# Performance work log

Hardware: AMD Instinct MI355X
Metric: run time of the kernel (lower is better)

Reference implementation:

```python
import jax, jax.numpy as jnp
import numpy as np

N = 20000
E = 640000
R = 8          # num_rels == num_bases (basis regularizer with num_bases=-1)
B = 8
IN_SIZE = 128
HID = 256      # 4 * fea_dimen
FEA = 64
TIME = 2880
POI = 12


def setup_inputs() -> dict:
    key = jax.random.key(0)
    ks = jax.random.split(key, 20)
    s = 0.02
    inp = {
        'src': jax.random.randint(ks[0], (E,), 0, N),
        'dst': jax.random.randint(ks[1], (E,), 0, N),
        'etype': jax.random.randint(ks[2], (E,), 0, R),
        'poi_distribution': jax.random.normal(ks[3], (N, POI), jnp.float32),
        'time_distribution': jax.random.normal(ks[4], (N, TIME), jnp.float32),
        'road_feature': jax.random.normal(ks[5], (N, IN_SIZE), jnp.float32),
        # input projections
        'poi_w': jax.random.normal(ks[6], (POI, FEA), jnp.float32) * s,
        'poi_b': jnp.zeros((FEA,), jnp.float32),
        'time_w': jax.random.normal(ks[7], (TIME, 2 * FEA), jnp.float32) * s,
        'time_b': jnp.zeros((2 * FEA,), jnp.float32),
        'road_w': jax.random.normal(ks[8], (IN_SIZE, FEA), jnp.float32) * s,
        'road_b': jnp.zeros((FEA,), jnp.float32),
        # RelGraphConv layer 1 (basis decomposition)
        'basis1': jax.random.normal(ks[9], (B, HID, HID), jnp.float32) * s,
        'coef1': jax.random.normal(ks[10], (R, B), jnp.float32) * s,
        'loop_w1': jax.random.normal(ks[11], (HID, HID), jnp.float32) * s,
        'bias1': jnp.zeros((HID,), jnp.float32),
        # RelGraphConv layer 2
        'basis2': jax.random.normal(ks[12], (B, HID, HID), jnp.float32) * s,
        'coef2': jax.random.normal(ks[13], (R, B), jnp.float32) * s,
        'loop_w2': jax.random.normal(ks[14], (HID, HID), jnp.float32) * s,
        'bias2': jnp.zeros((HID,), jnp.float32),
    }
    return inp


def _rel_graph_conv(h, src, dst, etype, basis, coef, loop_w, bias):
    # W_r = sum_b coef[r,b] * basis[b]  -> (R, HID, HID), small
    W = jnp.einsum('rb,bio->rio', coef, basis)
    # transform every node by every relation weight, then gather per edge
    y = jnp.einsum('ni,rio->nro', h, W)          # (N, R, HID)
    msgs = y[src, etype]                          # (E, HID) gather
    agg = jax.ops.segment_sum(msgs, dst, num_segments=h.shape[0])  # scatter-sum
    return agg + h @ loop_w + bias


def reference(src, dst, etype, poi_distribution, time_distribution, road_feature,
              poi_w, poi_b, time_w, time_b, road_w, road_b,
              basis1, coef1, loop_w1, bias1, basis2, coef2, loop_w2, bias2):
    poi_feat = poi_distribution @ poi_w + poi_b       # (N, 64)
    time_feat = time_distribution @ time_w + time_b   # (N, 128)
    road_feat = road_feature @ road_w + road_b        # (N, 64)
    feat = jnp.concatenate([poi_feat, time_feat, road_feat], axis=1)  # (N, 256)
    h = _rel_graph_conv(feat, src, dst, etype, basis1, coef1, loop_w1, bias1)
    h = jax.nn.relu(h)  # dropout=0.0 -> identity
    h = _rel_graph_conv(h, src, dst, etype, basis2, coef2, loop_w2, bias2)
    return h
```

## Files before the change

### kernel.cpp

```cpp
#include <hip/hip_runtime.h>

#define NN 20000
#define NE 640000
#define NR 8
#define NB 8
#define HID 256
#define KPOI 12
#define KTIME 2880
#define KROAD 128
#define NK (NN * NR)
#define NS 9
#define KCAT (NS * HID)

typedef __attribute__((ext_vector_type(8))) short bf8_t;
typedef __attribute__((ext_vector_type(4))) float f4_t;

__device__ inline unsigned short f2bf(float f) {
  unsigned int u = __float_as_uint(f);
  u += 0x7FFF + ((u >> 16) & 1);
  return (unsigned short)(u >> 16);
}
__device__ inline float bf2f(unsigned short h) {
  return __uint_as_float((unsigned int)h << 16);
}

__device__ inline void gl_lds16(const void* g, void* l) {
  __builtin_amdgcn_global_load_lds(
      (const __attribute__((address_space(1))) void*)g,
      (__attribute__((address_space(3))) void*)l, 16, 0, 0);
}

#define BK 16
__device__ inline void sgemm_body(
    int M, int Nn, int K,
    const float* __restrict__ A, int lda,
    const float* __restrict__ B, int ldb,
    const float* __restrict__ bias,
    unsigned short* __restrict__ C, int ldc, int brow, char* lds)
{
  constexpr int BM = 64, BN = 64, TM = 4, TN = 4;
  constexpr int SA = BM + 4;
  constexpr int SB = BN + 4;
  float* As = (float*)lds;
  float* Bs = (float*)(lds + 4352);
  const int tid = threadIdx.x;
  constexpr int TCOLS = BN / TN;
  const int row0 = (tid / TCOLS) * TM;
  const int col0 = (tid % TCOLS) * TN;

  float acc[TM][TN] = {};

  for (int kb = 0; kb < K; kb += BK) {
    {
      int i = tid;
      int r = i >> 2, q = (i & 3) * 4;
      int grow = brow + r, gk = kb + q;
      if (grow < M && gk + 3 < K) {
        float4 v = *(const float4*)(A + (size_t)grow * lda + gk);
        As[(q + 0) * SA + r] = v.x;
        As[(q + 1) * SA + r] = v.y;
        As[(q + 2) * SA + r] = v.z;
        As[(q + 3) * SA + r] = v.w;
      } else {
#pragma unroll
        for (int j = 0; j < 4; ++j)
          As[(q + j) * SA + r] =
              (grow < M && gk + j < K) ? A[(size_t)grow * lda + gk + j] : 0.f;
      }
    }
    {
      int i = tid;
      int k = i / (BN / 4), cq = (i % (BN / 4)) * 4;
      int gk = kb + k;
      float4 v = {0.f, 0.f, 0.f, 0.f};
      if (gk < K) {
        if (cq + 3 < Nn) {
          v = *(const float4*)(B + (size_t)gk * ldb + cq);
        } else {
#pragma unroll
          for (int j = 0; j < 4; ++j)
            if (cq + j < Nn) (&v.x)[j] = B[(size_t)gk * ldb + cq + j];
        }
      }
      *(float4*)(&Bs[k * SB + cq]) = v;
    }
    __syncthreads();
#pragma unroll
    for (int kk = 0; kk < BK; ++kk) {
      float a[TM], bb[TN];
      *(float4*)(&a[0]) = *(const float4*)(&As[kk * SA + row0]);
      *(float4*)(&bb[0]) = *(const float4*)(&Bs[kk * SB + col0]);
#pragma unroll
      for (int i = 0; i < TM; ++i)
#pragma unroll
        for (int j = 0; j < TN; ++j)
          acc[i][j] += a[i] * bb[j];
    }
    __syncthreads();
  }

  float bcache[TN];
#pragma unroll
  for (int j = 0; j < TN; ++j) bcache[j] = bias[col0 + j];
#pragma unroll
  for (int i = 0; i < TM; ++i) {
    int row = brow + row0 + i;
    if (row >= M) continue;
#pragma unroll
    for (int j = 0; j < TN; ++j)
      C[(size_t)row * ldc + col0 + j] = f2bf(acc[i][j] + bcache[j]);
  }
}

__global__ __launch_bounds__(256) void hist_prep_k(
    const int* __restrict__ dstp, const int* __restrict__ etp,
    int* __restrict__ counts,
    const float* __restrict__ loop_w1, const float* __restrict__ loop_w2,
    const float* __restrict__ time_w,
    const float* __restrict__ coef1, const float* __restrict__ basis1,
    const float* __restrict__ coef2, const float* __restrict__ basis2,
    const float* __restrict__ poi_dist, const float* __restrict__ poi_w,
    const float* __restrict__ poi_b,
    const float* __restrict__ road_feat, const float* __restrict__ road_w,
    const float* __restrict__ road_b,
    unsigned short* __restrict__ Wc1, unsigned short* __restrict__ Wc2,
    unsigned short* __restrict__ TWT, unsigned short* __restrict__ hbuf)
{
  __shared__ __align__(16) char lds[8704];
  int b = blockIdx.x;
  if (b < 2500) {
    int e = b * 256 + threadIdx.x;
    atomicAdd(&counts[dstp[e] * NR + etp[e]], 1);
    return;
  }
  b -= 2500;
  const int to = threadIdx.x & 63;
  const int tq = threadIdx.x >> 6;

  if (b < 378) {
    unsigned short (*T)[66] = (unsigned short (*)[66])lds;
    if (b < 256) {
      const int lr = b >> 4;
      const int tile = b & 15;
      const int i0 = ((tile >> 2) & 3) * 64, o0 = (tile & 3) * 64;
      const float* coef  = (lr < NR) ? coef1 : coef2;
      const float* basis = (lr < NR) ? basis1 : basis2;
      unsigned short* Wc = (lr < NR) ? Wc1 : Wc2;
      const int r = lr & 7;
      float cf[NB];
#pragma unroll
      for (int q = 0; q < NB; ++q) cf[q] = coef[r * NB + q];
#pragma unroll
      for (int k = 0; k < 16; ++k) {
        int i_loc = tq * 16 + k;
        int i = i0 + i_loc;
        float acc = 0.f;
#pragma unroll
        for (int q = 0; q < NB; ++q)
          acc += cf[q] * basis[((size_t)(q * HID + i)) * HID + o0 + to];
        T[i_loc][to] = f2bf(acc);
      }
      __syncthreads();
#pragma unroll
      for (int k = 0; k < 16; ++k) {
        int o_loc = tq * 16 + k;
        Wc[(size_t)(o0 + o_loc) * KCAT + r * HID + i0 + to] = T[to][o_loc];
      }
    } else if (b < 288) {
      const int j = b - 256;
      const int layer = j >> 4;
      const int tile = j & 15;
      const int i0 = ((tile >> 2) & 3) * 64, o0 = (tile & 3) * 64;
      const float* lw = layer ? loop_w2 : loop_w1;
      unsigned short* Wc = layer ? Wc2 : Wc1;
#pragma unroll
      for (int k = 0; k < 16; ++k) {
        int i_loc = tq * 16 + k;
        T[i_loc][to] = f2bf(lw[(size_t)(i0 + i_loc) * HID + o0 + to]);
      }
      __syncthreads();
#pragma unroll
      for (int k = 0; k < 16; ++k) {
        int o_loc = tq * 16 + k;
        Wc[(size_t)(o0 + o_loc) * KCAT + NR * HID + i0 + to] = T[to][o_loc];
      }
    } else {
      const int j = b - 288;
      const int r0 = (j >> 1) * 64, c0 = (j & 1) * 64;
#pragma unroll
      for (int k = 0; k < 16; ++k) {
        int r_loc = tq * 16 + k;
        T[r_loc][to] = f2bf(time_w[(size_t)(r0 + r_loc) * 128 + c0 + to]);
      }
      __syncthreads();
#pragma unroll
      for (int k = 0; k < 16; ++k) {
        int c_loc = tq * 16 + k;
        TWT[(size_t)(c0 + c_loc) * KTIME + r0 + to] = T[to][c_loc];
      }
    }
  } else if (b < 691) {
    sgemm_body(NN, 64, KPOI, poi_dist, KPOI, poi_w, 64, poi_b,
               hbuf + 0, HID, (b - 378) * 64, lds);
  } else {
    sgemm_body(NN, 64, KROAD, road_feat, KROAD, road_w, 64, road_b,
               hbuf + 192, HID, (b - 691) * 64, lds);
  }
}

__global__ __launch_bounds__(256) void scan_all(
    const int* __restrict__ counts, int* __restrict__ offs,
    int* __restrict__ cursor, int* __restrict__ bsums,
    int* __restrict__ counter) {
  __shared__ int sh[256];
  const int bid = blockIdx.x;
  const int t = threadIdx.x;
  const int nblk = gridDim.x;
  const int gbase = bid * 1024;
  int v[4], run[4];
  int s = 0;
#pragma unroll
  for (int j = 0; j < 4; ++j) {
    int idx = gbase + t * 4 + j;
    v[j] = (idx < NK) ? counts[idx] : 0;
    s += v[j];
  }
  sh[t] = s;
  __syncthreads();
  for (int off = 1; off < 256; off <<= 1) {
    int x = (t >= off) ? sh[t - off] : 0;
    __syncthreads();
    sh[t] += x;
    __syncthreads();
  }
  {
    int r = sh[t] - s;
#pragma unroll
    for (int j = 0; j < 4; ++j) { run[j] = r; r += v[j]; }
  }
  if (t == 255) {
    bsums[bid] = sh[255];
    __threadfence();
    atomicAdd(counter, 1);
  }
  if (t == 0) {
    while (atomicAdd(counter, 0) < nblk) {}
    __threadfence();
  }
  __syncthreads();
  int bs = (t < nblk) ? atomicAdd(&bsums[t], 0) : 0;
  __syncthreads();
  sh[t] = bs;
  __syncthreads();
  for (int off = 1; off < 256; off <<= 1) {
    int x = (t >= off) ? sh[t - off] : 0;
    __syncthreads();
    sh[t] += x;
    __syncthreads();
  }
  const int base = (bid > 0) ? sh[bid - 1] : 0;
#pragma unroll
  for (int j = 0; j < 4; ++j) {
    int idx = gbase + t * 4 + j;
    if (idx < NK) {
      int val = run[j] + base;
      offs[idx] = val;
      cursor[idx] = val;
    }
  }
  if (bid == 0 && t == 0) offs[NK] = NE;
}

__global__ __launch_bounds__(512) void fill_time_k(
    const int* __restrict__ srcp, const int* __restrict__ dstp,
    const int* __restrict__ etp, int* __restrict__ cursor,
    unsigned short* __restrict__ ssrc,
    const float* __restrict__ A,
    const unsigned short* __restrict__ BT,
    const float* __restrict__ bias,
    unsigned short* __restrict__ featb)
{
  __shared__ __align__(16) char lds[40960];
  int b = blockIdx.x;
  if (b < 1250) {
    int e = b * 512 + threadIdx.x;
    int key = dstp[e] * NR + etp[e];
    int p = atomicAdd(&cursor[key], 1);
    ssrc[p] = (unsigned short)srcp[e];
    return;
  }
  b -= 1250;
  char* ldsA = lds;
  char* ldsB = lds + 8192;
  const int tid = threadIdx.x;
  const int lane = tid & 63;
  const int w = tid >> 6;
  const int g = w >> 2;
  const int cb = w & 3;
  const int brow = b * 32;
  const int c8sw = (lane & 7) ^ (lane >> 3);

  f4_t acc[2][2];
#pragma unroll
  for (int i = 0; i < 2; ++i)
#pragma unroll
    for (int j = 0; j < 2; ++j) acc[i][j] = (f4_t){0.f, 0.f, 0.f, 0.f};

  for (int i = 0; i < 23; ++i) {
    {
      int sg = tid >> 8, r = (tid >> 3) & 31, c8 = tid & 7;
      int step = sg * 23 + i;
      unsigned short hh[8] = {0, 0, 0, 0, 0, 0, 0, 0};
      if (step < 45) {
        const float* ap = A + (size_t)(brow + r) * KTIME + step * 64 + c8 * 8;
        f4_t v0 = *(const f4_t*)ap;
        f4_t v1 = *(const f4_t*)(ap + 4);
#pragma unroll
        for (int j = 0; j < 4; ++j) { hh[j] = f2bf(v0[j]); hh[4 + j] = f2bf(v1[j]); }
      }
      *(bf8_t*)(ldsA + sg * 4096 + r * 128 + ((c8 * 16) ^ ((r & 7) << 4))) =
          *(bf8_t*)hh;
    }
#pragma unroll
    for (int it = 0; it < 4; ++it) {
      int s0 = (w << 6) + it * 512;
      int sg = s0 >> 10;
      int r0 = (s0 >> 3) & 127;
      int step = sg * 23 + i;
      if (step < 45) {
        int r = r0 + (lane >> 3);
        gl_lds16(BT + (size_t)r * KTIME + step * 64 + c8sw * 8,
                 ldsB + sg * 16384 + r0 * 128);
      }
    }
    __syncthreads();
    if (g * 23 + i < 45) {
#pragma unroll
      for (int ks = 0; ks < 2; ++ks) {
        const int kbyte = ks * 64 + (lane >> 4) * 16;
        bf8_t af[2], bfr[2];
#pragma unroll
        for (int mi = 0; mi < 2; ++mi) {
          int m = mi * 16 + (lane & 15);
          af[mi] = *(const bf8_t*)(
              ldsA + g * 4096 + m * 128 + (kbyte ^ ((m & 7) << 4)));
        }
#pragma unroll
        for (int ni = 0; ni < 2; ++ni) {
          int n = cb * 32 + ni * 16 + (lane & 15);
          bfr[ni] = *(const bf8_t*)(
              ldsB + g * 16384 + n * 128 + (kbyte ^ ((n & 7) << 4)));
        }
#pragma unroll
        for (int mi = 0; mi < 2; ++mi)
#pragma unroll
          for (int ni = 0; ni < 2; ++ni)
            acc[mi][ni] = __builtin_amdgcn_mfma_f32_16x16x32_bf16(
                af[mi], bfr[ni], acc[mi][ni], 0, 0, 0);
      }
    }
    __syncthreads();
  }

  float* rb = (float*)ldsB;
  if (g == 1) {
#pragma unroll
    for (int mi = 0; mi < 2; ++mi)
#pragma unroll
      for (int ni = 0; ni < 2; ++ni)
#pragma unroll
        for (int j = 0; j < 4; ++j)
          rb[(cb * 64 + lane) * 16 + (mi * 2 + ni) * 4 + j] = acc[mi][ni][j];
  }
  __syncthreads();
  if (g == 0) {
    const int rq = (lane >> 4) * 4;
    const int cl = lane & 15;
#pragma unroll
    for (int ni = 0; ni < 2; ++ni) {
      int c = cb * 32 + ni * 16 + cl;
      float bv = bias[c];
#pragma unroll
      for (int mi = 0; mi < 2; ++mi) {
#pragma unroll
        for (int j = 0; j < 4; ++j) {
          float v = acc[mi][ni][j] +
                    rb[(cb * 64 + lane) * 16 + (mi * 2 + ni) * 4 + j] + bv;
          int row = brow + mi * 16 + rq + j;
          featb[(size_t)row * 256 + 64 + c] = f2bf(v);
        }
      }
    }
  }
}

__global__ __launch_bounds__(256) void agg_k(
    const int* __restrict__ offs, const unsigned short* __restrict__ ssrc,
    const unsigned short* __restrict__ hin, unsigned short* __restrict__ Zc) {
  int d = (blockIdx.x * 256 + threadIdx.x) >> 6;
  int lane = threadIdx.x & 63;
  if (d >= NN) return;
  unsigned short* zrow = Zc + (size_t)d * KCAT;
  *(ushort4*)(zrow + NR * HID + lane * 4) =
      *(const ushort4*)(hin + (size_t)d * HID + lane * 4);
  int ob[NR + 1];
#pragma unroll
  for (int r = 0; r <= NR; ++r) ob[r] = offs[d * NR + r];
#pragma unroll 1
  for (int q = 0; q < NR; ++q) {
    int e = ob[q], hi = ob[q + 1];
    f4_t az = {0.f, 0.f, 0.f, 0.f};
    for (; e + 4 <= hi; e += 4) {
      int s0 = ssrc[e], s1 = ssrc[e + 1], s2 = ssrc[e + 2], s3 = ssrc[e + 3];
      ushort4 u0 = *(const ushort4*)(hin + (size_t)s0 * HID + lane * 4);
      ushort4 u1 = *(const ushort4*)(hin + (size_t)s1 * HID + lane * 4);
      ushort4 u2 = *(const ushort4*)(hin + (size_t)s2 * HID + lane * 4);
      ushort4 u3 = *(const ushort4*)(hin + (size_t)s3 * HID + lane * 4);
      az.x += (bf2f(u0.x) + bf2f(u1.x)) + (bf2f(u2.x) + bf2f(u3.x));
      az.y += (bf2f(u0.y) + bf2f(u1.y)) + (bf2f(u2.y) + bf2f(u3.y));
      az.z += (bf2f(u0.z) + bf2f(u1.z)) + (bf2f(u2.z) + bf2f(u3.z));
      az.w += (bf2f(u0.w) + bf2f(u1.w)) + (bf2f(u2.w) + bf2f(u3.w));
    }
    for (; e < hi; ++e) {
      int s = ssrc[e];
      ushort4 u = *(const ushort4*)(hin + (size_t)s * HID + lane * 4);
      az.x += bf2f(u.x); az.y += bf2f(u.y);
      az.z += bf2f(u.z); az.w += bf2f(u.w);
    }
    unsigned short hz[4] = {f2bf(az.x), f2bf(az.y), f2bf(az.z), f2bf(az.w)};
    *(ushort4*)(zrow + q * HID + lane * 4) = *(ushort4*)hz;
  }
}

template<int EPI>
__global__ __launch_bounds__(512) void gemm_cat(
    const unsigned short* __restrict__ Zc,
    const unsigned short* __restrict__ Wc,
    const float* __restrict__ bias,
    float* __restrict__ C, unsigned short* __restrict__ hb)
{
  __shared__ __align__(16) char At[64 * 128];
  __shared__ __align__(16) char Bt[256 * 128];
  const int tid = threadIdx.x;
  const int lane = tid & 63;
  const int w = tid >> 6;
  const int wm = w >> 2;
  const int wn = w & 3;
  const int brow = blockIdx.x * 64;
  const bool full = (brow + 64 <= NN);
  const int c8sw = (lane & 7) ^ (lane >> 3);

  f4_t acc[2][4];
#pragma unroll
  for (int i = 0; i < 2; ++i)
#pragma unroll
    for (int j = 0; j < 4; ++j) acc[i][j] = (f4_t){0.f, 0.f, 0.f, 0.f};

  for (int kb = 0; kb < KCAT; kb += 64) {
    if (full) {
      int row = (w << 3) + (lane >> 3);
      gl_lds16(Zc + (size_t)(brow + row) * KCAT + kb + c8sw * 8,
               At + (w << 10));
    } else {
      int r = tid >> 3, c8 = tid & 7;
      int grow = brow + r;
      bf8_t v = {0, 0, 0, 0, 0, 0, 0, 0};
      if (grow < NN) v = *(const bf8_t*)(Zc + (size_t)grow * KCAT + kb + c8 * 8);
      *(bf8_t*)(At + r * 128 + ((c8 * 16) ^ ((r & 7) << 4))) = v;
    }
#pragma unroll
    for (int it = 0; it < 4; ++it) {
      int n0 = (w << 3) + it * 64;
      int n = n0 + (lane >> 3);
      gl_lds16(Wc + (size_t)n * KCAT + kb + c8sw * 8, Bt + n0 * 128);
    }
    __syncthreads();
#pragma unroll
    for (int ks = 0; ks < 2; ++ks) {
      const int kbyte = ks * 64 + (lane >> 4) * 16;
      bf8_t af[2], bfr[4];
#pragma unroll
      for (int mi = 0; mi < 2; ++mi) {
        int m = wm * 32 + mi * 16 + (lane & 15);
        af[mi] = *(const bf8_t*)(At + m * 128 + (kbyte ^ ((m & 7) << 4)));
      }
#pragma unroll
      for (int ni = 0; ni < 4; ++ni) {
        int n = wn * 64 + ni * 16 + (lane & 15);
        bfr[ni] = *(const bf8_t*)(Bt + n * 128 + (kbyte ^ ((n & 7) << 4)));
      }
#pragma unroll
      for (int mi = 0; mi < 2; ++mi)
#pragma unroll
        for (int ni = 0; ni < 4; ++ni)
          acc[mi][ni] = __builtin_amdgcn_mfma_f32_16x16x32_bf16(
              af[mi], bfr[ni], acc[mi][ni], 0, 0, 0);
    }
    __syncthreads();
  }

  const int rq = (lane >> 4) * 4;
  const int cl = lane & 15;
#pragma unroll
  for (int ni = 0; ni < 4; ++ni) {
    int c = wn * 64 + ni * 16 + cl;
    float bv = bias[c];
#pragma unroll
    for (int mi = 0; mi < 2; ++mi) {
#pragma unroll
      for (int j = 0; j < 4; ++j) {
        int row = brow + wm * 32 + mi * 16 + rq + j;
        if (row < NN) {
          size_t o = (size_t)row * HID + c;
          float v = acc[mi][ni][j] + bv;
          if (EPI == 0) C[o] = v;
          else          hb[o] = f2bf(fmaxf(v, 0.f));
        }
      }
    }
  }
}

extern "C" void kernel_launch(void* const* d_in, const int* in_sizes, int n_in,
                              void* d_out, int out_size, void* d_ws, size_t ws_size,
                              hipStream_t stream) {
  const int*   srcp      = (const int*)d_in[0];
  const int*   dstp      = (const int*)d_in[1];
  const int*   etypep    = (const int*)d_in[2];
  const float* poi_dist  = (const float*)d_in[3];
  const float* time_dist = (const float*)d_in[4];
  const float* road_feat = (const float*)d_in[5];
  const float* poi_w     = (const float*)d_in[6];
  const float* poi_b     = (const float*)d_in[7];
  const float* time_w    = (const float*)d_in[8];
  const float* time_b    = (const float*)d_in[9];
  const float* road_w    = (const float*)d_in[10];
  const float* road_b    = (const float*)d_in[11];
  const float* basis1    = (const float*)d_in[12];
  const float* coef1     = (const float*)d_in[13];
  const float* loop_w1   = (const float*)d_in[14];
  const float* bias1     = (const float*)d_in[15];
  const float* basis2    = (const float*)d_in[16];
  const float* coef2     = (const float*)d_in[17];
  const float* loop_w2   = (const float*)d_in[18];
  const float* bias2     = (const float*)d_in[19];

  float* out = (float*)d_out;

  char* ws = (char*)d_ws;
  unsigned short* Wc1    = (unsigned short*)(ws);
  unsigned short* Wc2    = (unsigned short*)(ws + 1179648);
  unsigned short* TWT    = (unsigned short*)(ws + 2359296);
  unsigned short* hbuf   = (unsigned short*)(ws + 3096576);
  unsigned short* Zcat   = (unsigned short*)(ws + 13336576);
  int*            offs   = (int*)  (ws + 105496576);
  int*            bsums  = (int*)  (ws + 106136592);
  unsigned short* ssrc   = (unsigned short*)(ws + 106137616);
  int*            cursor = (int*)  (ws + 107417616);
  int*            counts = (int*)Zcat;
  int*            counter = counts + NK;

  dim3 blk(256);

  hipMemsetAsync(counts, 0, (NK + 1) * sizeof(int), stream);

  hist_prep_k<<<3504, blk, 0, stream>>>(dstp, etypep, counts,
                                        loop_w1, loop_w2, time_w,
                                        coef1, basis1, coef2, basis2,
                                        poi_dist, poi_w, poi_b,
                                        road_feat, road_w, road_b,
                                        Wc1, Wc2, TWT, hbuf);

  scan_all<<<(NK + 1023) / 1024, blk, 0, stream>>>(counts, offs, cursor,
                                                   bsums, counter);

  fill_time_k<<<1875, 512, 0, stream>>>(srcp, dstp, etypep, cursor, ssrc,
                                        time_dist, TWT, time_b, hbuf);

  agg_k<<<NN * 64 / 256, blk, 0, stream>>>(offs, ssrc, hbuf, Zcat);
  gemm_cat<1><<<(NN + 63) / 64, 512, 0, stream>>>(Zcat, Wc1, bias1, nullptr, hbuf);

  agg_k<<<NN * 64 / 256, blk, 0, stream>>>(offs, ssrc, hbuf, Zcat);
  gemm_cat<0><<<(NN + 63) / 64, 512, 0, stream>>>(Zcat, Wc2, bias2, out, nullptr);
}
```

Measured before the change: 379.8 us.

## Split edge fill from time projection and restructure time GEMM with small row tiles

Splits the fused edge-fill/time-projection kernel into two launches. The time projection now uses 11-row tiles: each block stages the full 2880-wide A rows into LDS as bf16, and each wave takes a strided share of the K steps. B fragments are read straight from global memory, and the per-wave partial sums are reduced through LDS float atomics. This aims to raise block count and parallelism over K and to drop the per-step syncs, but it wastes MFMA rows (11 of 16) and reads B from global without LDS reuse.

```diff
diff --git a/kernel.cpp b/kernel.cpp
--- a/kernel.cpp
+++ b/kernel.cpp
@@ -11,6 +11,8 @@
 #define NK (NN * NR)
 #define NS 9
 #define KCAT (NS * HID)
+#define TROWS 11
+#define TLROW 5776
 
 typedef __attribute__((ext_vector_type(8))) short bf8_t;
 typedef __attribute__((ext_vector_type(4))) float f4_t;
@@ -271,125 +273,84 @@
   if (bid == 0 && t == 0) offs[NK] = NE;
 }
 
-__global__ __launch_bounds__(512) void fill_time_k(
-    const int* __restrict__ srcp, const int* __restrict__ dstp,
-    const int* __restrict__ etp, int* __restrict__ cursor,
-    unsigned short* __restrict__ ssrc,
+__global__ __launch_bounds__(256) void fill_k(const int* __restrict__ src,
+                                              const int* __restrict__ dst,
+                                              const int* __restrict__ et,
+                                              int* __restrict__ cursor,
+                                              unsigned short* __restrict__ ssrc) {
+  int e = blockIdx.x * 256 + threadIdx.x;
+  if (e < NE) {
+    int key = dst[e] * NR + et[e];
+    int p = atomicAdd(&cursor[key], 1);
+    ssrc[p] = (unsigned short)src[e];
+  }
+}
+
+__global__ __launch_bounds__(512) void time_k(
     const float* __restrict__ A,
     const unsigned short* __restrict__ BT,
     const float* __restrict__ bias,
     unsigned short* __restrict__ featb)
 {
-  __shared__ __align__(16) char lds[40960];
-  int b = blockIdx.x;
-  if (b < 1250) {
-    int e = b * 512 + threadIdx.x;
-    int key = dstp[e] * NR + etp[e];
-    int p = atomicAdd(&cursor[key], 1);
-    ssrc[p] = (unsigned short)srcp[e];
-    return;
-  }
-  b -= 1250;
-  char* ldsA = lds;
-  char* ldsB = lds + 8192;
+  __shared__ __align__(16) char lds[TROWS * TLROW];
   const int tid = threadIdx.x;
   const int lane = tid & 63;
   const int w = tid >> 6;
-  const int g = w >> 2;
-  const int cb = w & 3;
-  const int brow = b * 32;
-  const int c8sw = (lane & 7) ^ (lane >> 3);
-
-  f4_t acc[2][2];
-#pragma unroll
-  for (int i = 0; i < 2; ++i)
-#pragma unroll
-    for (int j = 0; j < 2; ++j) acc[i][j] = (f4_t){0.f, 0.f, 0.f, 0.f};
-
-  for (int i = 0; i < 23; ++i) {
-    {
-      int sg = tid >> 8, r = (tid >> 3) & 31, c8 = tid & 7;
-      int step = sg * 23 + i;
-      unsigned short hh[8] = {0, 0, 0, 0, 0, 0, 0, 0};
-      if (step < 45) {
-        const float* ap = A + (size_t)(brow + r) * KTIME + step * 64 + c8 * 8;
-        f4_t v0 = *(const f4_t*)ap;
-        f4_t v1 = *(const f4_t*)(ap + 4);
-#pragma unroll
-        for (int j = 0; j < 4; ++j) { hh[j] = f2bf(v0[j]); hh[4 + j] = f2bf(v1[j]); }
-      }
-      *(bf8_t*)(ldsA + sg * 4096 + r * 128 + ((c8 * 16) ^ ((r & 7) << 4))) =
-          *(bf8_t*)hh;
-    }
-#pragma unroll
-    for (int it = 0; it < 4; ++it) {
-      int s0 = (w << 6) + it * 512;
-      int sg = s0 >> 10;
-      int r0 = (s0 >> 3) & 127;
-      int step = sg * 23 + i;
-      if (step < 45) {
-        int r = r0 + (lane >> 3);
-        gl_lds16(BT + (size_t)r * KTIME + step * 64 + c8sw * 8,
-                 ldsB + sg * 16384 + r0 * 128);
-      }
-    }
-    __syncthreads();
-    if (g * 23 + i < 45) {
-#pragma unroll
-      for (int ks = 0; ks < 2; ++ks) {
-        const int kbyte = ks * 64 + (lane >> 4) * 16;
-        bf8_t af[2], bfr[2];
-#pragma unroll
-        for (int mi = 0; mi < 2; ++mi) {
-          int m = mi * 16 + (lane & 15);
-          af[mi] = *(const bf8_t*)(
-              ldsA + g * 4096 + m * 128 + (kbyte ^ ((m & 7) << 4)));
-        }
-#pragma unroll
-        for (int ni = 0; ni < 2; ++ni) {
-          int n = cb * 32 + ni * 16 + (lane & 15);
-          bfr[ni] = *(const bf8_t*)(
-              ldsB + g * 16384 + n * 128 + (kbyte ^ ((n & 7) << 4)));
-        }
-#pragma unroll
-        for (int mi = 0; mi < 2; ++mi)
-#pragma unroll
-          for (int ni = 0; ni < 2; ++ni)
-            acc[mi][ni] = __builtin_amdgcn_mfma_f32_16x16x32_bf16(
-                af[mi], bfr[ni], acc[mi][ni], 0, 0, 0);
-      }
-    }
-    __syncthreads();
-  }
-
-  float* rb = (float*)ldsB;
-  if (g == 1) {
-#pragma unroll
-    for (int mi = 0; mi < 2; ++mi)
-#pragma unroll
-      for (int ni = 0; ni < 2; ++ni)
-#pragma unroll
-        for (int j = 0; j < 4; ++j)
-          rb[(cb * 64 + lane) * 16 + (mi * 2 + ni) * 4 + j] = acc[mi][ni][j];
-  }
-  __syncthreads();
-  if (g == 0) {
-    const int rq = (lane >> 4) * 4;
-    const int cl = lane & 15;
-#pragma unroll
-    for (int ni = 0; ni < 2; ++ni) {
-      int c = cb * 32 + ni * 16 + cl;
-      float bv = bias[c];
-#pragma unroll
-      for (int mi = 0; mi < 2; ++mi) {
-#pragma unroll
-        for (int j = 0; j < 4; ++j) {
-          float v = acc[mi][ni][j] +
-                    rb[(cb * 64 + lane) * 16 + (mi * 2 + ni) * 4 + j] + bv;
-          int row = brow + mi * 16 + rq + j;
-          featb[(size_t)row * 256 + 64 + c] = f2bf(v);
-        }
-      }
+  const int brow = blockIdx.x * TROWS;
+
+  const int CHUNKS = TROWS * 360;
+  for (int c = tid; c < CHUNKS; c += 512) {
+    int r = c / 360;
+    int k8 = (c - r * 360) * 8;
+    int grow = brow + r;
+    unsigned short hh[8] = {0, 0, 0, 0, 0, 0, 0, 0};
+    if (grow < NN) {
+      const float* ap = A + (size_t)grow * KTIME + k8;
+      f4_t v0 = *(const f4_t*)ap;
+      f4_t v1 = *(const f4_t*)(ap + 4);
+#pragma unroll
+      for (int j = 0; j < 4; ++j) { hh[j] = f2bf(v0[j]); hh[4 + j] = f2bf(v1[j]); }
+    }
+    *(bf8_t*)(lds + r * TLROW + k8 * 2) = *(bf8_t*)hh;
+  }
+  __syncthreads();
+
+  f4_t acc[8];
+#pragma unroll
+  for (int t = 0; t < 8; ++t) acc[t] = (f4_t){0.f, 0.f, 0.f, 0.f};
+  const int rA = lane & 15;
+  const int q8 = (lane >> 4) * 8;
+  for (int s = w; s < 90; s += 8) {
+    int koff = s * 32 + q8;
+    bf8_t af = *(const bf8_t*)(lds + rA * TLROW + koff * 2);
+#pragma unroll
+    for (int t = 0; t < 8; ++t) {
+      bf8_t bf = *(const bf8_t*)(BT + (size_t)(t * 16 + rA) * KTIME + koff);
+      acc[t] = __builtin_amdgcn_mfma_f32_16x16x32_bf16(af, bf, acc[t], 0, 0, 0);
+    }
+  }
+  __syncthreads();
+
+  float* P = (float*)lds;
+  if (tid < TROWS * 32) *(f4_t*)(P + tid * 4) = (f4_t){0.f, 0.f, 0.f, 0.f};
+  __syncthreads();
+  const int rq = (lane >> 4) * 4;
+#pragma unroll
+  for (int t = 0; t < 8; ++t)
+#pragma unroll
+    for (int j = 0; j < 4; ++j)
+      if (rq + j < TROWS)
+        atomicAdd(&P[(rq + j) * 128 + t * 16 + rA], acc[t][j]);
+  __syncthreads();
+  if (tid < TROWS * 32) {
+    int row = tid >> 5, c4 = (tid & 31) * 4;
+    int grow = brow + row;
+    if (grow < NN) {
+      f4_t v = *(const f4_t*)(P + row * 128 + c4);
+      f4_t b = *(const f4_t*)(bias + c4);
+      unsigned short h[4] = {f2bf(v.x + b.x), f2bf(v.y + b.y),
+                             f2bf(v.z + b.z), f2bf(v.w + b.w)};
+      *(ushort4*)(featb + (size_t)grow * 256 + 64 + c4) = *(ushort4*)h;
     }
   }
 }
@@ -574,8 +535,10 @@
   scan_all<<<(NK + 1023) / 1024, blk, 0, stream>>>(counts, offs, cursor,
                                                    bsums, counter);
 
-  fill_time_k<<<1875, 512, 0, stream>>>(srcp, dstp, etypep, cursor, ssrc,
-                                        time_dist, TWT, time_b, hbuf);
+  fill_k<<<(NE + 255) / 256, blk, 0, stream>>>(srcp, dstp, etypep, cursor, ssrc);
+
+  time_k<<<(NN + TROWS - 1) / TROWS, 512, 0, stream>>>(time_dist, TWT,
+                                                       time_b, hbuf);
 
   agg_k<<<NN * 64 / 256, blk, 0, stream>>>(offs, ssrc, hbuf, Zcat);
   gemm_cat<1><<<(NN + 63) / 64, 512, 0, stream>>>(Zcat, Wc1, bias1, nullptr, hbuf);
```

Result: slower. 620.9 us (+63.5%).

## Split time-projection GEMM into 5-way split-K with separate reduction kernel

Applied to the files above, without the earlier changes.

The time-distribution projection GEMM (20000x2880 by 2880x128) used to run as 625 blocks of 512 threads, each doing a 2-way in-block K split. It now runs as 5-way split-K over 3125 blocks of 256 threads, interleaved with the edge-fill blocks in the same launch. Partial sums are written in fp32 to the Zcat scratch buffer, and a new time_finish kernel adds them up, applies the bias and writes bf16. B-tile staging moves from async global_load_lds to plain vector loads. The aim is more parallelism and better overlap with the atomic fill work, paid for with extra partial-sum traffic and one more launch.

```diff
diff --git a/kernel.cpp b/kernel.cpp
--- a/kernel.cpp
+++ b/kernel.cpp
@@ -11,6 +11,8 @@
 #define NK (NN * NR)
 #define NS 9
 #define KCAT (NS * HID)
+#define SPLITK 5
+#define KCH (KTIME / SPLITK)
 
 typedef __attribute__((ext_vector_type(8))) short bf8_t;
 typedef __attribute__((ext_vector_type(4))) float f4_t;
@@ -271,34 +273,31 @@
   if (bid == 0 && t == 0) offs[NK] = NE;
 }
 
-__global__ __launch_bounds__(512) void fill_time_k(
+__global__ __launch_bounds__(256) void time_fill_k(
     const int* __restrict__ srcp, const int* __restrict__ dstp,
     const int* __restrict__ etp, int* __restrict__ cursor,
     unsigned short* __restrict__ ssrc,
     const float* __restrict__ A,
     const unsigned short* __restrict__ BT,
-    const float* __restrict__ bias,
-    unsigned short* __restrict__ featb)
+    float* __restrict__ TP)
 {
-  __shared__ __align__(16) char lds[40960];
-  int b = blockIdx.x;
-  if (b < 1250) {
-    int e = b * 512 + threadIdx.x;
+  __shared__ __align__(16) char lds[20480];
+  const int b = blockIdx.x;
+  const int grp = b / 9, rem = b % 9;
+  if (rem >= 5) {
+    int e = (grp * 4 + (rem - 5)) * 256 + threadIdx.x;
     int key = dstp[e] * NR + etp[e];
     int p = atomicAdd(&cursor[key], 1);
     ssrc[p] = (unsigned short)srcp[e];
     return;
   }
-  b -= 1250;
   char* ldsA = lds;
-  char* ldsB = lds + 8192;
+  char* ldsB = lds + 4096;
   const int tid = threadIdx.x;
   const int lane = tid & 63;
   const int w = tid >> 6;
-  const int g = w >> 2;
-  const int cb = w & 3;
-  const int brow = b * 32;
-  const int c8sw = (lane & 7) ^ (lane >> 3);
+  const int brow = grp * 32;
+  const int kb0 = rem * KCH;
 
   f4_t acc[2][2];
 #pragma unroll
@@ -306,92 +305,82 @@
 #pragma unroll
     for (int j = 0; j < 2; ++j) acc[i][j] = (f4_t){0.f, 0.f, 0.f, 0.f};
 
-  for (int i = 0; i < 23; ++i) {
+  for (int kb = kb0; kb < kb0 + KCH; kb += 64) {
     {
-      int sg = tid >> 8, r = (tid >> 3) & 31, c8 = tid & 7;
-      int step = sg * 23 + i;
-      unsigned short hh[8] = {0, 0, 0, 0, 0, 0, 0, 0};
-      if (step < 45) {
-        const float* ap = A + (size_t)(brow + r) * KTIME + step * 64 + c8 * 8;
-        f4_t v0 = *(const f4_t*)ap;
-        f4_t v1 = *(const f4_t*)(ap + 4);
-#pragma unroll
-        for (int j = 0; j < 4; ++j) { hh[j] = f2bf(v0[j]); hh[4 + j] = f2bf(v1[j]); }
-      }
-      *(bf8_t*)(ldsA + sg * 4096 + r * 128 + ((c8 * 16) ^ ((r & 7) << 4))) =
-          *(bf8_t*)hh;
+      int r = tid >> 3, c8 = tid & 7;
+      const float* ap = A + (size_t)(brow + r) * KTIME + kb + c8 * 8;
+      f4_t v0 = *(const f4_t*)ap;
+      f4_t v1 = *(const f4_t*)(ap + 4);
+      unsigned short hh[8];
+#pragma unroll
+      for (int j = 0; j < 4; ++j) { hh[j] = f2bf(v0[j]); hh[4 + j] = f2bf(v1[j]); }
+      *(bf8_t*)(ldsA + r * 128 + ((c8 * 16) ^ ((r & 7) << 4))) = *(bf8_t*)hh;
     }
 #pragma unroll
     for (int it = 0; it < 4; ++it) {
-      int s0 = (w << 6) + it * 512;
-      int sg = s0 >> 10;
-      int r0 = (s0 >> 3) & 127;
-      int step = sg * 23 + i;
-      if (step < 45) {
-        int r = r0 + (lane >> 3);
-        gl_lds16(BT + (size_t)r * KTIME + step * 64 + c8sw * 8,
-                 ldsB + sg * 16384 + r0 * 128);
-      }
-    }
-    __syncthreads();
-    if (g * 23 + i < 45) {
-#pragma unroll
-      for (int ks = 0; ks < 2; ++ks) {
-        const int kbyte = ks * 64 + (lane >> 4) * 16;
-        bf8_t af[2], bfr[2];
-#pragma unroll
-        for (int mi = 0; mi < 2; ++mi) {
-          int m = mi * 16 + (lane & 15);
-          af[mi] = *(const bf8_t*)(
-              ldsA + g * 4096 + m * 128 + (kbyte ^ ((m & 7) << 4)));
-        }
-#pragma unroll
-        for (int ni = 0; ni < 2; ++ni) {
-          int n = cb * 32 + ni * 16 + (lane & 15);
-          bfr[ni] = *(const bf8_t*)(
-              ldsB + g * 16384 + n * 128 + (kbyte ^ ((n & 7) << 4)));
-        }
-#pragma unroll
-        for (int mi = 0; mi < 2; ++mi)
-#pragma unroll
-          for (int ni = 0; ni < 2; ++ni)
-            acc[mi][ni] = __builtin_amdgcn_mfma_f32_16x16x32_bf16(
-                af[mi], bfr[ni], acc[mi][ni], 0, 0, 0);
-      }
-    }
-    __syncthreads();
-  }
-
-  float* rb = (float*)ldsB;
-  if (g == 1) {
-#pragma unroll
-    for (int mi = 0; mi < 2; ++mi)
-#pragma unroll
-      for (int ni = 0; ni < 2; ++ni)
-#pragma unroll
-        for (int j = 0; j < 4; ++j)
-          rb[(cb * 64 + lane) * 16 + (mi * 2 + ni) * 4 + j] = acc[mi][ni][j];
-  }
-  __syncthreads();
-  if (g == 0) {
-    const int rq = (lane >> 4) * 4;
-    const int cl = lane & 15;
-#pragma unroll
-    for (int ni = 0; ni < 2; ++ni) {
-      int c = cb * 32 + ni * 16 + cl;
-      float bv = bias[c];
+      int slot = tid + it * 256;
+      int r = slot >> 3, c8 = slot & 7;
+      bf8_t v = *(const bf8_t*)(BT + (size_t)r * KTIME + kb + c8 * 8);
+      *(bf8_t*)(ldsB + r * 128 + ((c8 * 16) ^ ((r & 7) << 4))) = v;
+    }
+    __syncthreads();
+#pragma unroll
+    for (int ks = 0; ks < 2; ++ks) {
+      const int kbyte = ks * 64 + (lane >> 4) * 16;
+      bf8_t af[2], bfr[2];
 #pragma unroll
       for (int mi = 0; mi < 2; ++mi) {
-#pragma unroll
-        for (int j = 0; j < 4; ++j) {
-          float v = acc[mi][ni][j] +
-                    rb[(cb * 64 + lane) * 16 + (mi * 2 + ni) * 4 + j] + bv;
-          int row = brow + mi * 16 + rq + j;
-          featb[(size_t)row * 256 + 64 + c] = f2bf(v);
-        }
-      }
-    }
-  }
+        int m = mi * 16 + (lane & 15);
+        af[mi] = *(const bf8_t*)(ldsA + m * 128 + (kbyte ^ ((m & 7) << 4)));
+      }
+#pragma unroll
+      for (int ni = 0; ni < 2; ++ni) {
+        int n = w * 32 + ni * 16 + (lane & 15);
+        bfr[ni] = *(const bf8_t*)(ldsB + n * 128 + (kbyte ^ ((n & 7) << 4)));
+      }
+#pragma unroll
+      for (int mi = 0; mi < 2; ++mi)
+#pragma unroll
+        for (int ni = 0; ni < 2; ++ni)
+          acc[mi][ni] = __builtin_amdgcn_mfma_f32_16x16x32_bf16(
+              af[mi], bfr[ni], acc[mi][ni], 0, 0, 0);
+    }
+    __syncthreads();
+  }
+
+  float* tp = TP + (size_t)rem * NN * 128;
+  const int rq = (lane >> 4) * 4;
+  const int cl = lane & 15;
+#pragma unroll
+  for (int ni = 0; ni < 2; ++ni) {
+    int c = w * 32 + ni * 16 + cl;
+#pragma unroll
+    for (int mi = 0; mi < 2; ++mi) {
+#pragma unroll
+      for (int j = 0; j < 4; ++j) {
+        int row = brow + mi * 16 + rq + j;
+        tp[(size_t)row * 128 + c] = acc[mi][ni][j];
+      }
+    }
+  }
+}
+
+__global__ __launch_bounds__(256) void time_finish(
+    const float* __restrict__ TP, const float* __restrict__ bias,
+    unsigned short* __restrict__ featb) {
+  int i = blockIdx.x * 256 + threadIdx.x;
+  if (i >= NN * 32) return;
+  int row = i >> 5, c4 = (i & 31) * 4;
+  f4_t s = *(const f4_t*)(TP + (size_t)row * 128 + c4);
+#pragma unroll
+  for (int k = 1; k < SPLITK; ++k) {
+    f4_t v = *(const f4_t*)(TP + (size_t)k * NN * 128 + (size_t)row * 128 + c4);
+    s.x += v.x; s.y += v.y; s.z += v.z; s.w += v.w;
+  }
+  f4_t b = *(const f4_t*)(bias + c4);
+  unsigned short h[4] = {f2bf(s.x + b.x), f2bf(s.y + b.y),
+                         f2bf(s.z + b.z), f2bf(s.w + b.w)};
+  *(ushort4*)(featb + (size_t)row * 256 + 64 + c4) = *(ushort4*)h;
 }
 
 __global__ __launch_bounds__(256) void agg_k(
@@ -559,6 +548,7 @@
   int*            cursor = (int*)  (ws + 107417616);
   int*            counts = (int*)Zcat;
   int*            counter = counts + NK;
+  float*          TP     = (float*)Zcat;
 
   dim3 blk(256);
 
@@ -574,8 +564,9 @@
   scan_all<<<(NK + 1023) / 1024, blk, 0, stream>>>(counts, offs, cursor,
                                                    bsums, counter);
 
-  fill_time_k<<<1875, 512, 0, stream>>>(srcp, dstp, etypep, cursor, ssrc,
-                                        time_dist, TWT, time_b, hbuf);
+  time_fill_k<<<5625, blk, 0, stream>>>(srcp, dstp, etypep, cursor, ssrc,
+                                        time_dist, TWT, TP);
+  time_finish<<<(NN * 32 + 255) / 256, blk, 0, stream>>>(TP, time_b, hbuf);
 
   agg_k<<<NN * 64 / 256, blk, 0, stream>>>(offs, ssrc, hbuf, Zcat);
   gemm_cat<1><<<(NN + 63) / 64, 512, 0, stream>>>(Zcat, Wc1, bias1, nullptr, hbuf);
```

After: 370.6 us. -2.4%, faster.
